# Optimization experiments

Measured on AMD Instinct MI355X. Metric: run time of the kernel, lower is better.

The kernel has to match this reference:

```python
import jax, jax.numpy as jnp
import numpy as np

N_NODES = 50000
N_EDGES = 400000
NUM_FEATURES = 32
NUM_GRAPHS = 64
NUM_CLASSES = 2


def setup_inputs() -> dict:
    key = jax.random.key(0)
    ks = jax.random.split(key, 24)
    inp = {
        "x": jax.random.normal(ks[0], (N_NODES, NUM_FEATURES), dtype=jnp.float32),
        "edge_index": jax.random.randint(ks[1], (2, N_EDGES), 0, N_NODES),
        "edge_attr": jax.random.uniform(ks[2], (N_EDGES, 1), dtype=jnp.float32),
        "batch": jnp.sort(jax.random.randint(ks[3], (N_NODES,), 0, NUM_GRAPHS)),
        # nn1: Linear(1,10) -> ReLU -> Linear(10, 32*16)
        "nn1_w1": jax.random.normal(ks[4], (1, 10), dtype=jnp.float32) * 0.3,
        "nn1_b1": jnp.zeros((10,), jnp.float32),
        "nn1_w2": jax.random.normal(ks[5], (10, NUM_FEATURES * 16), dtype=jnp.float32) * 0.1,
        "nn1_b2": jnp.zeros((NUM_FEATURES * 16,), jnp.float32),
        "conv1_root": jax.random.normal(ks[6], (NUM_FEATURES, 16), dtype=jnp.float32) * 0.1,
        "conv1_bias": jnp.zeros((16,), jnp.float32),
        # nn2: Linear(1,10) -> ReLU -> Linear(10, 16*32)
        "nn2_w1": jax.random.normal(ks[7], (1, 10), dtype=jnp.float32) * 0.3,
        "nn2_b1": jnp.zeros((10,), jnp.float32),
        "nn2_w2": jax.random.normal(ks[8], (10, 16 * 32), dtype=jnp.float32) * 0.1,
        "nn2_b2": jnp.zeros((16 * 32,), jnp.float32),
        "conv2_root": jax.random.normal(ks[9], (16, 32), dtype=jnp.float32) * 0.15,
        "conv2_bias": jnp.zeros((32,), jnp.float32),
        "fc1_w": jax.random.normal(ks[10], (32, 64), dtype=jnp.float32) * 0.15,
        "fc1_b": jnp.zeros((64,), jnp.float32),
        "fc2_w": jax.random.normal(ks[11], (64, NUM_CLASSES), dtype=jnp.float32) * 0.1,
        "fc2_b": jnp.zeros((NUM_CLASSES,), jnp.float32),
    }
    return inp


def _nnconv(x, edge_src, edge_dst, edge_attr, w1, b1, w2, b2, root, bias, in_ch, out_ch):
    # Per-edge weight matrix from edge MLP: [E, in_ch, out_ch]
    h = jax.nn.relu(edge_attr @ w1 + b1) @ w2 + b2
    W = h.reshape(-1, in_ch, out_ch)
    msg = jnp.einsum('ei,eio->eo', x[edge_src], W)  # [E, out_ch]
    agg = jax.ops.segment_sum(msg, edge_dst, num_segments=N_NODES)
    cnt = jax.ops.segment_sum(jnp.ones((msg.shape[0],), x.dtype), edge_dst, num_segments=N_NODES)
    mean = agg / jnp.maximum(cnt, 1.0)[:, None]
    return mean + x @ root + bias


def reference(x, edge_index, edge_attr, batch,
              nn1_w1, nn1_b1, nn1_w2, nn1_b2, conv1_root, conv1_bias,
              nn2_w1, nn2_b1, nn2_w2, nn2_b2, conv2_root, conv2_bias,
              fc1_w, fc1_b, fc2_w, fc2_b):
    src, dst = edge_index[0], edge_index[1]
    h = jax.nn.elu(_nnconv(x, src, dst, edge_attr, nn1_w1, nn1_b1, nn1_w2, nn1_b2,
                           conv1_root, conv1_bias, NUM_FEATURES, 16))
    h = jax.nn.elu(_nnconv(h, src, dst, edge_attr, nn2_w1, nn2_b1, nn2_w2, nn2_b2,
                           conv2_root, conv2_bias, 16, 32))
    # global mean pool over graphs
    gsum = jax.ops.segment_sum(h, batch, num_segments=NUM_GRAPHS)
    gcnt = jax.ops.segment_sum(jnp.ones((h.shape[0],), h.dtype), batch, num_segments=NUM_GRAPHS)
    g = gsum / jnp.maximum(gcnt, 1.0)[:, None]
    g = jax.nn.elu(g @ fc1_w + fc1_b)
    return jax.nn.log_softmax(g @ fc2_w + fc2_b, axis=1)
```

## Files before the change

### kernel.cpp

```cpp
#include <hip/hip_runtime.h>
#include <hip/hip_fp16.h>
#include <math.h>

#define N_NODES 50000
#define N_EDGES 400000
#define NUM_GRAPHS 64
#define NSCAN_BLK ((N_NODES + 1023) / 1024)


__global__ __launch_bounds__(256) void k0_hist(const int* __restrict__ src,
        const int* __restrict__ dst, int* __restrict__ deg, int* __restrict__ cntd) {
    int e = blockIdx.x * 256 + threadIdx.x;
    if (e < N_EDGES) {
        atomicAdd(deg + src[e], 1);
        atomicAdd(cntd + dst[e], 1);
    }
}

__global__ __launch_bounds__(1024) void k0_scanA(const int* __restrict__ deg,
        int* __restrict__ woff, int* __restrict__ bsum) {
    __shared__ int tmp[1024];
    int b = blockIdx.x, t = threadIdx.x;
    int n = b * 1024 + t;
    int v = (n < N_NODES) ? deg[n] : 0;
    tmp[t] = v;
    __syncthreads();
    for (int off = 1; off < 1024; off <<= 1) {
        int add = (t >= off) ? tmp[t - off] : 0;
        __syncthreads();
        tmp[t] += add;
        __syncthreads();
    }
    if (n < N_NODES) woff[n] = tmp[t] - v;
    if (t == 1023) bsum[b] = tmp[1023];
}

__global__ __launch_bounds__(1024) void k0_scanB(const int* __restrict__ bsum,
        int* __restrict__ woff) {
    __shared__ int boff;
    int b = blockIdx.x, t = threadIdx.x;
    if (t == 0) {
        int s = 0;
        for (int i = 0; i < b; i++) s += bsum[i];
        boff = s;
    }
    __syncthreads();
    int n = b * 1024 + t;
    if (n < N_NODES) woff[n] += boff;
}

__global__ __launch_bounds__(256) void k0_scatter(const int* __restrict__ src,
        const int* __restrict__ dst, const float* __restrict__ ea,
        int* __restrict__ woff, int* __restrict__ ses, int* __restrict__ sed,
        float* __restrict__ sea) {
    int e = blockIdx.x * 256 + threadIdx.x;
    if (e < N_EDGES) {
        int s = src[e];
        int pos = atomicAdd(woff + s, 1);
        ses[pos] = s;
        sed[pos] = dst[e];
        sea[pos] = ea[e];
    }
}

__global__ __launch_bounds__(256) void k1_p1(const float* __restrict__ x,
        const float* __restrict__ w2, const float* __restrict__ b2,
        const float* __restrict__ root, __half* __restrict__ P,
        float* __restrict__ R1) {
    __shared__ float Wl[32][192];
    __shared__ float xl[16][32];
    int t = threadIdx.x;
    for (int idx = t; idx < 32 * 192; idx += 256) {
        int i = idx / 192, c = idx % 192;
        int m = c >> 4, o = c & 15;
        float w;
        if (m < 10)       w = w2[m * 512 + i * 16 + o];
        else if (m == 10) w = b2[i * 16 + o];
        else              w = root[i * 16 + o];
        Wl[i][c] = w;
    }
    int n0 = blockIdx.x * 16;
    for (int idx = t; idx < 16 * 32; idx += 256) {
        int nl = idx >> 5, i = idx & 31;
        int n = n0 + nl;
        xl[nl][i] = (n < N_NODES) ? x[n * 32 + i] : 0.f;
    }
    __syncthreads();
    int nl = t >> 4, o = t & 15;
    int n = n0 + nl;
    if (n >= N_NODES) return;
    float acc[12];
#pragma unroll
    for (int m = 0; m < 12; m++) acc[m] = 0.f;
#pragma unroll
    for (int i = 0; i < 32; i++) {
        float xv = xl[nl][i];
#pragma unroll
        for (int m = 0; m < 12; m++) acc[m] += xv * Wl[i][m * 16 + o];
    }
    __half2* Po = (__half2*)(P + (size_t)n * 192 + o * 12);
#pragma unroll
    for (int k = 0; k < 6; k++) Po[k] = __floats2half2_rn(acc[2 * k], acc[2 * k + 1]);
    R1[n * 16 + o] = acc[11];
}

__global__ __launch_bounds__(256) void k4_p2(const float* __restrict__ agg1,
        const int* __restrict__ cntd, const float* __restrict__ R1,
        const float* __restrict__ bias1,
        const float* __restrict__ w2, const float* __restrict__ b2,
        const float* __restrict__ root, __half* __restrict__ P2,
        float* __restrict__ R2) {
    __shared__ float Wl[16][384];
    __shared__ float hl[8][16];
    int t = threadIdx.x;
    for (int idx = t; idx < 16 * 384; idx += 256) {
        int i = idx / 384, c = idx % 384;
        int m = c >> 5, o = c & 31;
        float w;
        if (m < 10)       w = w2[m * 512 + i * 32 + o];
        else if (m == 10) w = b2[i * 32 + o];
        else              w = root[i * 32 + o];
        Wl[i][c] = w;
    }
    int n0 = blockIdx.x * 8;
    if (t < 128) {
        int nl = t >> 4, i = t & 15;
        int n = n0 + nl;
        float v = 0.f;
        if (n < N_NODES) {
            int ci = cntd[n];
            float c = (float)(ci > 0 ? ci : 1);
            v = agg1[n * 16 + i] / c + R1[n * 16 + i] + bias1[i];
            v = v > 0.f ? v : expm1f(v);
        }
        hl[nl][i] = v;
    }
    __syncthreads();
    int nl = t >> 5, o = t & 31;
    int n = n0 + nl;
    if (n >= N_NODES) return;
    float acc[12];
#pragma unroll
    for (int m = 0; m < 12; m++) acc[m] = 0.f;
#pragma unroll
    for (int i = 0; i < 16; i++) {
        float hv = hl[nl][i];
#pragma unroll
        for (int m = 0; m < 12; m++) acc[m] += hv * Wl[i][m * 32 + o];
    }
    __half2* Po = (__half2*)(P2 + (size_t)n * 384 + o * 12);
#pragma unroll
    for (int k = 0; k < 6; k++) Po[k] = __floats2half2_rn(acc[2 * k], acc[2 * k + 1]);
    R2[(size_t)n * 32 + o] = acc[11];
}

__global__ __launch_bounds__(256) void k2_edge1(const __half* __restrict__ P,
        const int* __restrict__ ses, const int* __restrict__ sed,
        const float* __restrict__ sea, const float* __restrict__ w1,
        const float* __restrict__ b1, float* __restrict__ agg) {
    int t = threadIdx.x;
    int e = blockIdx.x * 16 + (t >> 4);
    int o = t & 15;
    if (e >= N_EDGES) return;
    float a = sea[e];
    int s = ses[e], d = sed[e];
    const float2* Pf = (const float2*)P;
    int base = s * 48 + o * 3;
    float2 f0 = Pf[base];
    float2 f1 = Pf[base + 1];
    float2 f2 = Pf[base + 2];
    float r[10];
#pragma unroll
    for (int j = 0; j < 10; j++) r[j] = fmaxf(a * w1[j] + b1[j], 0.f);
    union { float2 f; __half2 h[2]; } u;
    float m;
    {
        u.f = f2;
        float2 p89 = __half22float2(u.h[0]);
        float2 pQR = __half22float2(u.h[1]);
        m = pQR.x + r[8] * p89.x + r[9] * p89.y;
    }
    {
        u.f = f0;
        float2 p01 = __half22float2(u.h[0]);
        float2 p23 = __half22float2(u.h[1]);
        m += r[0] * p01.x + r[1] * p01.y + r[2] * p23.x + r[3] * p23.y;
    }
    {
        u.f = f1;
        float2 p45 = __half22float2(u.h[0]);
        float2 p67 = __half22float2(u.h[1]);
        m += r[4] * p45.x + r[5] * p45.y + r[6] * p67.x + r[7] * p67.y;
    }
    atomicAdd(agg + d * 16 + o, m);
}

__global__ __launch_bounds__(256) void k5_edge2(const __half* __restrict__ P,
        const int* __restrict__ ses, const int* __restrict__ sed,
        const float* __restrict__ sea, const float* __restrict__ w1,
        const float* __restrict__ b1, float* __restrict__ agg) {
    int t = threadIdx.x;
    int e = blockIdx.x * 8 + (t >> 5);
    int o = t & 31;
    if (e >= N_EDGES) return;
    float a = sea[e];
    int s = ses[e], d = sed[e];
    const float2* Pf = (const float2*)P;
    int base = s * 96 + o * 3;
    float2 f0 = Pf[base];
    float2 f1 = Pf[base + 1];
    float2 f2 = Pf[base + 2];
    float r[10];
#pragma unroll
    for (int j = 0; j < 10; j++) r[j] = fmaxf(a * w1[j] + b1[j], 0.f);
    union { float2 f; __half2 h[2]; } u;
    float m;
    {
        u.f = f2;
        float2 p89 = __half22float2(u.h[0]);
        float2 pQR = __half22float2(u.h[1]);
        m = pQR.x + r[8] * p89.x + r[9] * p89.y;
    }
    {
        u.f = f0;
        float2 p01 = __half22float2(u.h[0]);
        float2 p23 = __half22float2(u.h[1]);
        m += r[0] * p01.x + r[1] * p01.y + r[2] * p23.x + r[3] * p23.y;
    }
    {
        u.f = f1;
        float2 p45 = __half22float2(u.h[0]);
        float2 p67 = __half22float2(u.h[1]);
        m += r[4] * p45.x + r[5] * p45.y + r[6] * p67.x + r[7] * p67.y;
    }
    atomicAdd(agg + d * 32 + o, m);
}

__global__ __launch_bounds__(256) void k6_partial(const float* __restrict__ agg2,
        const int* __restrict__ cntd, const float* __restrict__ R2,
        const float* __restrict__ bias2, const int* __restrict__ batch,
        float* __restrict__ gsum) {
    const int NB = 512;
    const int chunk = (N_NODES + NB - 1) / NB;
    int begin = blockIdx.x * chunk;
    int end = begin + chunk;
    if (end > N_NODES) end = N_NODES;
    int t = threadIdx.x;
    int o = t & 31, ch = t >> 5;
    float bz = bias2[o];
    float acc = 0.f;
    int cur_g = -1;
    for (int n = begin + ch; n < end; n += 8) {
        int g = batch[n];
        int ci = cntd[n];
        float c = (float)(ci > 0 ? ci : 1);
        float v = agg2[(size_t)n * 32 + o] / c + R2[(size_t)n * 32 + o] + bz;
        v = v > 0.f ? v : expm1f(v);
        if (g != cur_g) {
            if (cur_g >= 0) atomicAdd(gsum + cur_g * 32 + o, acc);
            cur_g = g; acc = 0.f;
        }
        acc += v;
    }
    if (cur_g >= 0) atomicAdd(gsum + cur_g * 32 + o, acc);
}

__global__ __launch_bounds__(256) void k8_head(const float* __restrict__ gsum,
        const int* __restrict__ batch,
        const float* __restrict__ fc1w, const float* __restrict__ fc1b,
        const float* __restrict__ fc2w, const float* __restrict__ fc2b,
        float* __restrict__ out) {
    __shared__ float gl[64][32];
    __shared__ float w1l[32][64];
    __shared__ float hl[64][64];
    __shared__ float zl[64][2];
    __shared__ float gc[64];
    int t = threadIdx.x;
    if (t < 64) {
        int g = t;
        int lo = 0, hi = N_NODES;
        while (lo < hi) { int mid = (lo + hi) >> 1; if (batch[mid] < g) lo = mid + 1; else hi = mid; }
        int s0 = lo;
        lo = 0; hi = N_NODES;
        while (lo < hi) { int mid = (lo + hi) >> 1; if (batch[mid] < g + 1) lo = mid + 1; else hi = mid; }
        gc[g] = fmaxf((float)(lo - s0), 1.0f);
    }
    for (int idx = t; idx < 32 * 64; idx += 256) w1l[idx >> 6][idx & 63] = fc1w[idx];
    __syncthreads();
    for (int idx = t; idx < 64 * 32; idx += 256) gl[idx >> 5][idx & 31] = gsum[idx] / gc[idx >> 5];
    __syncthreads();
    for (int idx = t; idx < 64 * 64; idx += 256) {
        int gg = idx >> 6, c = idx & 63;
        float acc = fc1b[c];
#pragma unroll
        for (int i = 0; i < 32; i++) acc += gl[gg][i] * w1l[i][c];
        hl[gg][c] = acc > 0.f ? acc : expm1f(acc);
    }
    __syncthreads();
    if (t < 128) {
        int gg = t >> 1, k = t & 1;
        float acc = fc2b[k];
#pragma unroll
        for (int c = 0; c < 64; c++) acc += hl[gg][c] * fc2w[c * 2 + k];
        zl[gg][k] = acc;
    }
    __syncthreads();
    if (t < 128) {
        int gg = t >> 1, k = t & 1;
        float z0 = zl[gg][0], z1 = zl[gg][1];
        float m = fmaxf(z0, z1);
        float lse = m + logf(expf(z0 - m) + expf(z1 - m));
        out[t] = zl[gg][k] - lse;
    }
}

extern "C" void kernel_launch(void* const* d_in, const int* in_sizes, int n_in,
                              void* d_out, int out_size, void* d_ws, size_t ws_size,
                              hipStream_t stream) {
    const float* x       = (const float*)d_in[0];
    const int*   ei      = (const int*)d_in[1];
    const float* ea      = (const float*)d_in[2];
    const int*   batch   = (const int*)d_in[3];
    const float* nn1_w1  = (const float*)d_in[4];
    const float* nn1_b1  = (const float*)d_in[5];
    const float* nn1_w2  = (const float*)d_in[6];
    const float* nn1_b2  = (const float*)d_in[7];
    const float* c1_root = (const float*)d_in[8];
    const float* c1_bias = (const float*)d_in[9];
    const float* nn2_w1  = (const float*)d_in[10];
    const float* nn2_b1  = (const float*)d_in[11];
    const float* nn2_w2  = (const float*)d_in[12];
    const float* nn2_b2  = (const float*)d_in[13];
    const float* c2_root = (const float*)d_in[14];
    const float* c2_bias = (const float*)d_in[15];
    const float* fc1w    = (const float*)d_in[16];
    const float* fc1b    = (const float*)d_in[17];
    const float* fc2w    = (const float*)d_in[18];
    const float* fc2b    = (const float*)d_in[19];
    const int* src = ei;
    const int* dst = ei + N_EDGES;

    char* ws = (char*)d_ws;
    size_t off = 0;
    __half* P1 = (__half*)(ws + off); off += (size_t)N_NODES * 192 * 2;
    __half* P2 = (__half*)(ws + off); off += (size_t)N_NODES * 384 * 2;
    float* R1  = (float*)(ws + off);  off += (size_t)N_NODES * 16 * 4;
    float* R2  = (float*)(ws + off);  off += (size_t)N_NODES * 32 * 4;
    char* zbase = ws + off;
    int*   deg  = (int*)(ws + off);   off += (size_t)N_NODES * 4;
    int*   cntd = (int*)(ws + off);   off += (size_t)N_NODES * 4;
    float* agg1 = (float*)(ws + off); off += (size_t)N_NODES * 16 * 4;
    float* agg2 = (float*)(ws + off); off += (size_t)N_NODES * 32 * 4;
    float* gsum = (float*)(ws + off); off += (size_t)NUM_GRAPHS * 32 * 4;
    size_t zbytes = (size_t)(ws + off - zbase);
    int*   woff = (int*)(ws + off);   off += (size_t)N_NODES * 4;
    int*   bsum = (int*)(ws + off);   off += (size_t)NSCAN_BLK * 4;
    int*   ses  = (int*)(ws + off);   off += (size_t)N_EDGES * 4;
    int*   sed  = (int*)(ws + off);   off += (size_t)N_EDGES * 4;
    float* sea  = (float*)(ws + off); off += (size_t)N_EDGES * 4;

    hipMemsetAsync(zbase, 0, zbytes, stream);

    k0_hist<<<(N_EDGES + 255) / 256, 256, 0, stream>>>(src, dst, deg, cntd);
    k0_scanA<<<NSCAN_BLK, 1024, 0, stream>>>(deg, woff, bsum);
    k0_scanB<<<NSCAN_BLK, 1024, 0, stream>>>(bsum, woff);
    k0_scatter<<<(N_EDGES + 255) / 256, 256, 0, stream>>>(src, dst, ea, woff, ses, sed, sea);
    k1_p1<<<(N_NODES + 15) / 16, 256, 0, stream>>>(x, nn1_w2, nn1_b2, c1_root, P1, R1);
    k2_edge1<<<(N_EDGES + 15) / 16, 256, 0, stream>>>(P1, ses, sed, sea, nn1_w1, nn1_b1, agg1);
    k4_p2<<<(N_NODES + 7) / 8, 256, 0, stream>>>(agg1, cntd, R1, c1_bias, nn2_w2, nn2_b2, c2_root, P2, R2);
    k5_edge2<<<(N_EDGES + 7) / 8, 256, 0, stream>>>(P2, ses, sed, sea, nn2_w1, nn2_b1, agg2);
    k6_partial<<<512, 256, 0, stream>>>(agg2, cntd, R2, c2_bias, batch, gsum);
    k8_head<<<1, 256, 0, stream>>>(gsum, batch, fc1w, fc1b, fc2w, fc2b, (float*)d_out);
}
```

Measured before the change: 321.3 us.

## Precompute per-node piecewise-linear tables by ReLU interval and switch to CSR gather

Result: slower. 334.9 us (+4.2%).

```diff
diff --git a/kernel.cpp b/kernel.cpp
--- a/kernel.cpp
+++ b/kernel.cpp
@@ -8,21 +8,53 @@
 #define NSCAN_BLK ((N_NODES + 1023) / 1024)
 
 
-__global__ __launch_bounds__(256) void k0_hist(const int* __restrict__ src,
-        const int* __restrict__ dst, int* __restrict__ deg, int* __restrict__ cntd) {
+__global__ void k_thr(const float* __restrict__ w1a, const float* __restrict__ b1a,
+                      const float* __restrict__ w1b, const float* __restrict__ b1b,
+                      float* __restrict__ T, int* __restrict__ M) {
+    if (threadIdx.x != 0 || blockIdx.x != 0) return;
+    for (int layer = 0; layer < 2; layer++) {
+        const float* w1 = layer ? w1b : w1a;
+        const float* b1 = layer ? b1b : b1a;
+        float t[10]; int idx[10];
+        for (int j = 0; j < 10; j++) {
+            float w = w1[j];
+            t[j] = (w != 0.f) ? (-b1[j] / w) : INFINITY;
+            idx[j] = j;
+        }
+        for (int i = 1; i < 10; i++) {
+            float tv = t[i]; int iv = idx[i]; int k = i - 1;
+            while (k >= 0 && t[k] > tv) { t[k + 1] = t[k]; idx[k + 1] = idx[k]; k--; }
+            t[k + 1] = tv; idx[k + 1] = iv;
+        }
+        int pos[10];
+        for (int k = 0; k < 10; k++) pos[idx[k]] = k;
+        for (int k = 0; k < 10; k++) T[layer * 10 + k] = t[k];
+        for (int kap = 0; kap <= 10; kap++) {
+            int m = 0;
+            for (int j = 0; j < 10; j++) {
+                float w = w1[j];
+                bool act = (w > 0.f) ? (pos[j] < kap)
+                         : (w < 0.f) ? (pos[j] >= kap)
+                         : (b1[j] > 0.f);
+                if (act) m |= (1 << j);
+            }
+            M[layer * 11 + kap] = m;
+        }
+    }
+}
+
+__global__ __launch_bounds__(256) void k0_hist(const int* __restrict__ dst,
+        int* __restrict__ cntd) {
     int e = blockIdx.x * 256 + threadIdx.x;
-    if (e < N_EDGES) {
-        atomicAdd(deg + src[e], 1);
-        atomicAdd(cntd + dst[e], 1);
-    }
-}
-
-__global__ __launch_bounds__(1024) void k0_scanA(const int* __restrict__ deg,
-        int* __restrict__ woff, int* __restrict__ bsum) {
+    if (e < N_EDGES) atomicAdd(cntd + dst[e], 1);
+}
+
+__global__ __launch_bounds__(1024) void k0_scanA(const int* __restrict__ cntd,
+        int* __restrict__ roff, int* __restrict__ woff, int* __restrict__ bsum) {
     __shared__ int tmp[1024];
     int b = blockIdx.x, t = threadIdx.x;
     int n = b * 1024 + t;
-    int v = (n < N_NODES) ? deg[n] : 0;
+    int v = (n < N_NODES) ? cntd[n] : 0;
     tmp[t] = v;
     __syncthreads();
     for (int off = 1; off < 1024; off <<= 1) {
@@ -31,12 +63,12 @@
         tmp[t] += add;
         __syncthreads();
     }
-    if (n < N_NODES) woff[n] = tmp[t] - v;
+    if (n < N_NODES) { int ex = tmp[t] - v; roff[n] = ex; woff[n] = ex; }
     if (t == 1023) bsum[b] = tmp[1023];
 }
 
 __global__ __launch_bounds__(1024) void k0_scanB(const int* __restrict__ bsum,
-        int* __restrict__ woff) {
+        int* __restrict__ roff, int* __restrict__ woff) {
     __shared__ int boff;
     int b = blockIdx.x, t = threadIdx.x;
     if (t == 0) {
@@ -46,29 +78,39 @@
     }
     __syncthreads();
     int n = b * 1024 + t;
-    if (n < N_NODES) woff[n] += boff;
+    if (n < N_NODES) { roff[n] += boff; woff[n] += boff; }
 }
 
 __global__ __launch_bounds__(256) void k0_scatter(const int* __restrict__ src,
         const int* __restrict__ dst, const float* __restrict__ ea,
-        int* __restrict__ woff, int* __restrict__ ses, int* __restrict__ sed,
-        float* __restrict__ sea) {
+        const float* __restrict__ T, int* __restrict__ woff,
+        int* __restrict__ sse1, int* __restrict__ sse2, float* __restrict__ sea) {
     int e = blockIdx.x * 256 + threadIdx.x;
-    if (e < N_EDGES) {
-        int s = src[e];
-        int pos = atomicAdd(woff + s, 1);
-        ses[pos] = s;
-        sed[pos] = dst[e];
-        sea[pos] = ea[e];
-    }
+    if (e >= N_EDGES) return;
+    int s = src[e], d = dst[e];
+    float a = ea[e];
+    int k1 = 0, k2 = 0;
+#pragma unroll
+    for (int j = 0; j < 10; j++) {
+        k1 += (T[j] < a);
+        k2 += (T[10 + j] < a);
+    }
+    int pos = atomicAdd(woff + d, 1);
+    sse1[pos] = s * 11 + k1;
+    sse2[pos] = s * 11 + k2;
+    sea[pos] = a;
 }
 
 __global__ __launch_bounds__(256) void k1_p1(const float* __restrict__ x,
         const float* __restrict__ w2, const float* __restrict__ b2,
-        const float* __restrict__ root, __half* __restrict__ P,
+        const float* __restrict__ root, const float* __restrict__ w1,
+        const float* __restrict__ b1, const float* __restrict__ bias1,
+        const int* __restrict__ M, __half2* __restrict__ tab1,
         float* __restrict__ R1) {
     __shared__ float Wl[32][192];
     __shared__ float xl[16][32];
+    __shared__ float w1l[10], b1l[10];
+    __shared__ int ml[11];
     int t = threadIdx.x;
     for (int idx = t; idx < 32 * 192; idx += 256) {
         int i = idx / 192, c = idx % 192;
@@ -79,6 +121,8 @@
         else              w = root[i * 16 + o];
         Wl[i][c] = w;
     }
+    if (t < 10) { w1l[t] = w1[t]; b1l[t] = b1[t]; }
+    if (t < 11) ml[t] = M[t];
     int n0 = blockIdx.x * 16;
     for (int idx = t; idx < 16 * 32; idx += 256) {
         int nl = idx >> 5, i = idx & 31;
@@ -98,20 +142,54 @@
 #pragma unroll
         for (int m = 0; m < 12; m++) acc[m] += xv * Wl[i][m * 16 + o];
     }
-    __half2* Po = (__half2*)(P + (size_t)n * 192 + o * 12);
-#pragma unroll
-    for (int k = 0; k < 6; k++) Po[k] = __floats2half2_rn(acc[2 * k], acc[2 * k + 1]);
-    R1[n * 16 + o] = acc[11];
-}
-
-__global__ __launch_bounds__(256) void k4_p2(const float* __restrict__ agg1,
-        const int* __restrict__ cntd, const float* __restrict__ R1,
-        const float* __restrict__ bias1,
+#pragma unroll
+    for (int kap = 0; kap <= 10; kap++) {
+        int m = ml[kap];
+        float A = 0.f, B = acc[10];
+#pragma unroll
+        for (int j = 0; j < 10; j++) {
+            float f = ((m >> j) & 1) ? 1.f : 0.f;
+            A += f * w1l[j] * acc[j];
+            B += f * b1l[j] * acc[j];
+        }
+        tab1[((size_t)(n * 11 + kap)) * 16 + o] = __floats2half2_rn(A, B);
+    }
+    R1[n * 16 + o] = acc[11] + bias1[o];
+}
+
+__global__ __launch_bounds__(256) void k2_edge1(const __half2* __restrict__ tab1,
+        const int* __restrict__ roff, const int* __restrict__ sse1,
+        const float* __restrict__ sea, const float* __restrict__ R1,
+        float* __restrict__ h1) {
+    int t = threadIdx.x;
+    int d = blockIdx.x * 16 + (t >> 4);
+    int o = t & 15;
+    if (d >= N_NODES) return;
+    int start = roff[d];
+    int end = (d == N_NODES - 1) ? N_EDGES : roff[d + 1];
+    float acc = 0.f;
+    for (int p = start; p < end; ++p) {
+        int row = sse1[p];
+        float a = sea[p];
+        float2 f = __half22float2(tab1[(size_t)row * 16 + o]);
+        acc += a * f.x + f.y;
+    }
+    int deg = end - start;
+    float c = (float)(deg > 0 ? deg : 1);
+    float v = acc / c + R1[d * 16 + o];
+    h1[d * 16 + o] = v > 0.f ? v : expm1f(v);
+}
+
+__global__ __launch_bounds__(256) void k4_p2(const float* __restrict__ h1,
         const float* __restrict__ w2, const float* __restrict__ b2,
-        const float* __restrict__ root, __half* __restrict__ P2,
+        const float* __restrict__ root, const float* __restrict__ w1,
+        const float* __restrict__ b1, const float* __restrict__ bias2,
+        const int* __restrict__ M, __half2* __restrict__ tab2,
         float* __restrict__ R2) {
     __shared__ float Wl[16][384];
     __shared__ float hl[8][16];
+    __shared__ float w1l[10], b1l[10];
+    __shared__ int ml[11];
     int t = threadIdx.x;
     for (int idx = t; idx < 16 * 384; idx += 256) {
         int i = idx / 384, c = idx % 384;
@@ -122,18 +200,13 @@
         else              w = root[i * 32 + o];
         Wl[i][c] = w;
     }
+    if (t < 10) { w1l[t] = w1[t]; b1l[t] = b1[t]; }
+    if (t < 11) ml[t] = M[11 + t];
     int n0 = blockIdx.x * 8;
     if (t < 128) {
         int nl = t >> 4, i = t & 15;
         int n = n0 + nl;
-        float v = 0.f;
-        if (n < N_NODES) {
-            int ci = cntd[n];
-            float c = (float)(ci > 0 ? ci : 1);
-            v = agg1[n * 16 + i] / c + R1[n * 16 + i] + bias1[i];
-            v = v > 0.f ? v : expm1f(v);
-        }
-        hl[nl][i] = v;
+        hl[nl][i] = (n < N_NODES) ? h1[n * 16 + i] : 0.f;
     }
     __syncthreads();
     int nl = t >> 5, o = t & 31;
@@ -148,98 +221,46 @@
 #pragma unroll
         for (int m = 0; m < 12; m++) acc[m] += hv * Wl[i][m * 32 + o];
     }
-    __half2* Po = (__half2*)(P2 + (size_t)n * 384 + o * 12);
-#pragma unroll
-    for (int k = 0; k < 6; k++) Po[k] = __floats2half2_rn(acc[2 * k], acc[2 * k + 1]);
-    R2[(size_t)n * 32 + o] = acc[11];
-}
-
-__global__ __launch_bounds__(256) void k2_edge1(const __half* __restrict__ P,
-        const int* __restrict__ ses, const int* __restrict__ sed,
-        const float* __restrict__ sea, const float* __restrict__ w1,
-        const float* __restrict__ b1, float* __restrict__ agg) {
-    int t = threadIdx.x;
-    int e = blockIdx.x * 16 + (t >> 4);
-    int o = t & 15;
-    if (e >= N_EDGES) return;
-    float a = sea[e];
-    int s = ses[e], d = sed[e];
-    const float2* Pf = (const float2*)P;
-    int base = s * 48 + o * 3;
-    float2 f0 = Pf[base];
-    float2 f1 = Pf[base + 1];
-    float2 f2 = Pf[base + 2];
-    float r[10];
-#pragma unroll
-    for (int j = 0; j < 10; j++) r[j] = fmaxf(a * w1[j] + b1[j], 0.f);
-    union { float2 f; __half2 h[2]; } u;
-    float m;
-    {
-        u.f = f2;
-        float2 p89 = __half22float2(u.h[0]);
-        float2 pQR = __half22float2(u.h[1]);
-        m = pQR.x + r[8] * p89.x + r[9] * p89.y;
-    }
-    {
-        u.f = f0;
-        float2 p01 = __half22float2(u.h[0]);
-        float2 p23 = __half22float2(u.h[1]);
-        m += r[0] * p01.x + r[1] * p01.y + r[2] * p23.x + r[3] * p23.y;
-    }
-    {
-        u.f = f1;
-        float2 p45 = __half22float2(u.h[0]);
-        float2 p67 = __half22float2(u.h[1]);
-        m += r[4] * p45.x + r[5] * p45.y + r[6] * p67.x + r[7] * p67.y;
-    }
-    atomicAdd(agg + d * 16 + o, m);
-}
-
-__global__ __launch_bounds__(256) void k5_edge2(const __half* __restrict__ P,
-        const int* __restrict__ ses, const int* __restrict__ sed,
-        const float* __restrict__ sea, const float* __restrict__ w1,
-        const float* __restrict__ b1, float* __restrict__ agg) {
-    int t = threadIdx.x;
-    int e = blockIdx.x * 8 + (t >> 5);
+#pragma unroll
+    for (int kap = 0; kap <= 10; kap++) {
+        int m = ml[kap];
+        float A = 0.f, B = acc[10];
+#pragma unroll
+        for (int j = 0; j < 10; j++) {
+            float f = ((m >> j) & 1) ? 1.f : 0.f;
+            A += f * w1l[j] * acc[j];
+            B += f * b1l[j] * acc[j];
+        }
+        tab2[((size_t)(n * 11 + kap)) * 32 + o] = __floats2half2_rn(A, B);
+    }
+    R2[(size_t)n * 32 + o] = acc[11] + bias2[o];
+}
+
+__global__ __launch_bounds__(256) void k5_edge2(const __half2* __restrict__ tab2,
+        const int* __restrict__ roff, const int* __restrict__ sse2,
+        const float* __restrict__ sea, const float* __restrict__ R2,
+        float* __restrict__ h2) {
+    int t = threadIdx.x;
+    int d = blockIdx.x * 8 + (t >> 5);
     int o = t & 31;
-    if (e >= N_EDGES) return;
-    float a = sea[e];
-    int s = ses[e], d = sed[e];
-    const float2* Pf = (const float2*)P;
-    int base = s * 96 + o * 3;
-    float2 f0 = Pf[base];
-    float2 f1 = Pf[base + 1];
-    float2 f2 = Pf[base + 2];
-    float r[10];
-#pragma unroll
-    for (int j = 0; j < 10; j++) r[j] = fmaxf(a * w1[j] + b1[j], 0.f);
-    union { float2 f; __half2 h[2]; } u;
-    float m;
-    {
-        u.f = f2;
-        float2 p89 = __half22float2(u.h[0]);
-        float2 pQR = __half22float2(u.h[1]);
-        m = pQR.x + r[8] * p89.x + r[9] * p89.y;
-    }
-    {
-        u.f = f0;
-        float2 p01 = __half22float2(u.h[0]);
-        float2 p23 = __half22float2(u.h[1]);
-        m += r[0] * p01.x + r[1] * p01.y + r[2] * p23.x + r[3] * p23.y;
-    }
-    {
-        u.f = f1;
-        float2 p45 = __half22float2(u.h[0]);
-        float2 p67 = __half22float2(u.h[1]);
-        m += r[4] * p45.x + r[5] * p45.y + r[6] * p67.x + r[7] * p67.y;
-    }
-    atomicAdd(agg + d * 32 + o, m);
-}
-
-__global__ __launch_bounds__(256) void k6_partial(const float* __restrict__ agg2,
-        const int* __restrict__ cntd, const float* __restrict__ R2,
-        const float* __restrict__ bias2, const int* __restrict__ batch,
-        float* __restrict__ gsum) {
+    if (d >= N_NODES) return;
+    int start = roff[d];
+    int end = (d == N_NODES - 1) ? N_EDGES : roff[d + 1];
+    float acc = 0.f;
+    for (int p = start; p < end; ++p) {
+        int row = sse2[p];
+        float a = sea[p];
+        float2 f = __half22float2(tab2[(size_t)row * 32 + o]);
+        acc += a * f.x + f.y;
+    }
+    int deg = end - start;
+    float c = (float)(deg > 0 ? deg : 1);
+    float v = acc / c + R2[(size_t)d * 32 + o];
+    h2[(size_t)d * 32 + o] = v > 0.f ? v : expm1f(v);
+}
+
+__global__ __launch_bounds__(256) void k6_partial(const float* __restrict__ h2,
+        const int* __restrict__ batch, float* __restrict__ gsum) {
     const int NB = 512;
     const int chunk = (N_NODES + NB - 1) / NB;
     int begin = blockIdx.x * chunk;
@@ -247,15 +268,11 @@
     if (end > N_NODES) end = N_NODES;
     int t = threadIdx.x;
     int o = t & 31, ch = t >> 5;
-    float bz = bias2[o];
     float acc = 0.f;
     int cur_g = -1;
     for (int n = begin + ch; n < end; n += 8) {
         int g = batch[n];
-        int ci = cntd[n];
-        float c = (float)(ci > 0 ? ci : 1);
-        float v = agg2[(size_t)n * 32 + o] / c + R2[(size_t)n * 32 + o] + bz;
-        v = v > 0.f ? v : expm1f(v);
+        float v = h2[(size_t)n * 32 + o];
         if (g != cur_g) {
             if (cur_g >= 0) atomicAdd(gsum + cur_g * 32 + o, acc);
             cur_g = g; acc = 0.f;
@@ -342,33 +359,39 @@
 
     char* ws = (char*)d_ws;
     size_t off = 0;
-    __half* P1 = (__half*)(ws + off); off += (size_t)N_NODES * 192 * 2;
-    __half* P2 = (__half*)(ws + off); off += (size_t)N_NODES * 384 * 2;
-    float* R1  = (float*)(ws + off);  off += (size_t)N_NODES * 16 * 4;
-    float* R2  = (float*)(ws + off);  off += (size_t)N_NODES * 32 * 4;
+    __half2* tab1 = (__half2*)(ws + off); off += (size_t)N_NODES * 11 * 16 * 4;
+    __half2* tab2 = (__half2*)(ws + off); off += (size_t)N_NODES * 11 * 32 * 4;
+    float* R1   = (float*)(ws + off); off += (size_t)N_NODES * 16 * 4;
+    float* R2   = (float*)(ws + off); off += (size_t)N_NODES * 32 * 4;
+    float* h1   = (float*)(ws + off); off += (size_t)N_NODES * 16 * 4;
+    float* h2   = (float*)(ws + off); off += (size_t)N_NODES * 32 * 4;
+    int*   roff = (int*)(ws + off);   off += (size_t)N_NODES * 4;
+    int*   woff = (int*)(ws + off);   off += (size_t)N_NODES * 4;
+    int*   bsum = (int*)(ws + off);   off += (size_t)NSCAN_BLK * 4;
+    int*   sse1 = (int*)(ws + off);   off += (size_t)N_EDGES * 4;
+    int*   sse2 = (int*)(ws + off);   off += (size_t)N_EDGES * 4;
+    float* sea  = (float*)(ws + off); off += (size_t)N_EDGES * 4;
+    float* thrT = (float*)(ws + off); off += 20 * 4;
+    int*   thrM = (int*)(ws + off);   off += 22 * 4;
+    off = (off + 255) & ~(size_t)255;
     char* zbase = ws + off;
-    int*   deg  = (int*)(ws + off);   off += (size_t)N_NODES * 4;
     int*   cntd = (int*)(ws + off);   off += (size_t)N_NODES * 4;
-    float* agg1 = (float*)(ws + off); off += (size_t)N_NODES * 16 * 4;
-    float* agg2 = (float*)(ws + off); off += (size_t)N_NODES * 32 * 4;
     float* gsum = (float*)(ws + off); off += (size_t)NUM_GRAPHS * 32 * 4;
     size_t zbytes = (size_t)(ws + off - zbase);
-    int*   woff = (int*)(ws + off);   off += (size_t)N_NODES * 4;
-    int*   bsum = (int*)(ws + off);   off += (size_t)NSCAN_BLK * 4;
-    int*   ses  = (int*)(ws + off);   off += (size_t)N_EDGES * 4;
-    int*   sed  = (int*)(ws + off);   off += (size_t)N_EDGES * 4;
-    float* sea  = (float*)(ws + off); off += (size_t)N_EDGES * 4;
 
     hipMemsetAsync(zbase, 0, zbytes, stream);
 
-    k0_hist<<<(N_EDGES + 255) / 256, 256, 0, stream>>>(src, dst, deg, cntd);
-    k0_scanA<<<NSCAN_BLK, 1024, 0, stream>>>(deg, woff, bsum);
-    k0_scanB<<<NSCAN_BLK, 1024, 0, stream>>>(bsum, woff);
-    k0_scatter<<<(N_EDGES + 255) / 256, 256, 0, stream>>>(src, dst, ea, woff, ses, sed, sea);
-    k1_p1<<<(N_NODES + 15) / 16, 256, 0, stream>>>(x, nn1_w2, nn1_b2, c1_root, P1, R1);
-    k2_edge1<<<(N_EDGES + 15) / 16, 256, 0, stream>>>(P1, ses, sed, sea, nn1_w1, nn1_b1, agg1);
-    k4_p2<<<(N_NODES + 7) / 8, 256, 0, stream>>>(agg1, cntd, R1, c1_bias, nn2_w2, nn2_b2, c2_root, P2, R2);
-    k5_edge2<<<(N_EDGES + 7) / 8, 256, 0, stream>>>(P2, ses, sed, sea, nn2_w1, nn2_b1, agg2);
-    k6_partial<<<512, 256, 0, stream>>>(agg2, cntd, R2, c2_bias, batch, gsum);
+    k_thr<<<1, 64, 0, stream>>>(nn1_w1, nn1_b1, nn2_w1, nn2_b1, thrT, thrM);
+    k0_hist<<<(N_EDGES + 255) / 256, 256, 0, stream>>>(dst, cntd);
+    k0_scanA<<<NSCAN_BLK, 1024, 0, stream>>>(cntd, roff, woff, bsum);
+    k0_scanB<<<NSCAN_BLK, 1024, 0, stream>>>(bsum, roff, woff);
+    k0_scatter<<<(N_EDGES + 255) / 256, 256, 0, stream>>>(src, dst, ea, thrT, woff, sse1, sse2, sea);
+    k1_p1<<<(N_NODES + 15) / 16, 256, 0, stream>>>(x, nn1_w2, nn1_b2, c1_root,
+            nn1_w1, nn1_b1, c1_bias, thrM, tab1, R1);
+    k2_edge1<<<(N_NODES + 15) / 16, 256, 0, stream>>>(tab1, roff, sse1, sea, R1, h1);
+    k4_p2<<<(N_NODES + 7) / 8, 256, 0, stream>>>(h1, nn2_w2, nn2_b2, c2_root,
+            nn2_w1, nn2_b1, c2_bias, thrM, tab2, R2);
+    k5_edge2<<<(N_NODES + 7) / 8, 256, 0, stream>>>(tab2, roff, sse2, sea, R2, h2);
+    k6_partial<<<512, 256, 0, stream>>>(h2, batch, gsum);
     k8_head<<<1, 256, 0, stream>>>(gsum, batch, fc1w, fc1b, fc2w, fc2b, (float*)d_out);
 }
```
